# Performance work log

Measured on AMD Instinct MI355X. Metric: run time of the kernel, lower is better.

Reference implementation:

```python
import jax, jax.numpy as jnp
import numpy as np

NUM_CAV = 62000            # CAVs in the ragged batch
K = 3                      # past frames per object


def _counts():
    # deterministic ragged counts in [1, 31]; sum = 2000 * 496 = 992000 objects
    return ((np.arange(NUM_CAV) % 31) + 1).astype(np.int32)


def setup_inputs() -> dict:
    key = jax.random.key(0)
    k1, k2 = jax.random.split(key)
    counts = _counts()
    n_obj = int(counts.sum())  # 992000
    # [N, 3, 7] past 7-dof boxes; only [..., :2] (x, y) is used
    past_k_object_bbx = jax.random.normal(k1, (n_obj, K, 7), dtype=jnp.float32) * 10.0
    # strictly increasing timestamps per CAV so frame-to-frame dt != 0
    dt = jax.random.uniform(k2, (NUM_CAV, K), dtype=jnp.float32, minval=0.05, maxval=0.2)
    past_k_time_interval = jnp.cumsum(dt, axis=1).reshape(-1)  # flat, view(-1,3) compatible
    past_k_object_cav_num = jnp.asarray(counts)
    return {
        'past_k_object_bbx': past_k_object_bbx,
        'past_k_time_interval': past_k_time_interval,
        'past_k_object_cav_num': past_k_object_cav_num,
    }


def reference(past_k_object_bbx, past_k_time_interval, past_k_object_cav_num):
    # Faithful vectorization of extract_date_backup1 (j-indexed replicate loop ==
    # repeat_interleave of per-CAV time rows to per-object rows).
    n_obj = past_k_object_bbx.shape[0]
    # time grid per CAV, reversed so index -1 is the most recent frame
    td = jnp.flip(past_k_time_interval.reshape(-1, K), axis=1)        # [C, 3]
    coords = jnp.flip(past_k_object_bbx[:, :, :2], axis=1)           # [N, 3, 2]
    coords = coords - coords[:, -1:, :]                               # normalize to last frame
    # ragged row replication -> gather via cumulative offsets
    offsets = jnp.cumsum(past_k_object_cav_num)                       # [C]
    cav_idx = jnp.searchsorted(offsets, jnp.arange(n_obj), side='right')
    td_rep = td[cav_idx]                                              # [N, 3]
    td_norm = td_rep - td_rep[:, -1:]                                  # [N, 3]
    dt = td_rep[:, 1:] - td_rep[:, :-1]                                # [N, 2] (time_encode)
    distance = coords[:, 1:, :] - coords[:, :-1, :]                    # [N, 2, 2]
    speed = distance / dt[..., None]                                   # [N, 2, 2]
    obj_input = jnp.concatenate([distance, speed], axis=-1)[None]      # [1, N, 2, 4]
    # linear extrapolation of last motion to t = 0 (the 'query')
    last_len = td_norm[:, -1] - td_norm[:, -2]                          # [N]
    safe_len = jnp.where(last_len == 0, jnp.float32(1.0), last_len)
    extrap = coords[:, -1, :] + (coords[:, -1, :] - coords[:, -2, :]) * (-td_rep[:, -1:]) / safe_len[:, None]
    query = jnp.where((last_len == 0)[:, None], jnp.float32(0.0), extrap).reshape(1, n_obj, 1, 2)
    target_time_diff = -td_rep[:, -1]                                  # [N]
    time_encode = dt                                                   # [N, 2]
    return obj_input, query, time_encode, target_time_diff
```

## Files before the change

### kernel.cpp

```cpp
#include <hip/hip_runtime.h>
#include <limits.h>
#include <stdint.h>

#define SCAN_BS 1024
#define OBJ_PER 512
#define OBJ_BS  512
#define SLAB_F  (OBJ_PER * 21)
#define WIN     513
#define SOFF_CH 9

__device__ __forceinline__ void gload_lds16(const void* g, void* l) {
    __builtin_amdgcn_global_load_lds(
        (const __attribute__((address_space(1))) uint32_t*)g,
        (__attribute__((address_space(3))) uint32_t*)l, 16, 0, 0);
}
__device__ __forceinline__ void gload_lds4(const void* g, void* l) {
    __builtin_amdgcn_global_load_lds(
        (const __attribute__((address_space(1))) uint32_t*)g,
        (__attribute__((address_space(3))) uint32_t*)l, 4, 0, 0);
}


__global__ __launch_bounds__(SCAN_BS) void scan_fused_kernel(
    const int* __restrict__ counts, int C,
    int* __restrict__ flags, int* __restrict__ offsets, int* __restrict__ blockCav) {

    __shared__ int sdata[SCAN_BS];
    __shared__ int carry_s;
    const int b = blockIdx.x;
    const int tid = threadIdx.x;
    const int gid = b * SCAN_BS + tid;
    const int v = (gid < C) ? counts[gid] : 0;

    sdata[tid] = v;
    __syncthreads();
    for (int ofs = 1; ofs < SCAN_BS; ofs <<= 1) {
        int add = (tid >= ofs) ? sdata[tid - ofs] : 0;
        __syncthreads();
        sdata[tid] += add;
        __syncthreads();
    }

    if (tid == SCAN_BS - 1)
        __hip_atomic_store(&flags[b], sdata[SCAN_BS - 1] + 1,
                           __ATOMIC_RELEASE, __HIP_MEMORY_SCOPE_AGENT);

    if (tid < 64) {
        int sum = 0;
        for (int p = tid; p < b; p += 64) {
            int f;
            do {
                f = __hip_atomic_load(&flags[p], __ATOMIC_ACQUIRE, __HIP_MEMORY_SCOPE_AGENT);
            } while (f == 0);
            sum += f - 1;
        }
        #pragma unroll
        for (int o = 32; o > 0; o >>= 1) sum += __shfl_down(sum, o, 64);
        if (tid == 0) carry_s = sum;
    }
    __syncthreads();

    if (gid < C) {
        const int end = sdata[tid] + carry_s;
        offsets[gid] = end;
        const int start = end - v;
        int s0 = ((start + OBJ_PER - 1) / OBJ_PER) * OBJ_PER;
        for (int s = s0; s < end; s += OBJ_PER) blockCav[s / OBJ_PER] = gid;
    }
}


__global__ __launch_bounds__(OBJ_BS) void motion_kernel(
    const float* __restrict__ bbx, const float* __restrict__ tint,
    const int* __restrict__ offsets, const int* __restrict__ blockCav,
    int C, int N, float* __restrict__ out) {

    __shared__ __align__(16) float sb[SLAB_F];
    __shared__ int soff[SOFF_CH * 64];

    const int tid  = threadIdx.x;
    const int lane = tid & 63;
    const int wid  = tid >> 6;
    const long long blockStart = (long long)blockIdx.x * OBJ_PER;
    const int nObjBlk = (int)min((long long)OBJ_PER, (long long)N - blockStart);

    const int c_lo = blockCav[blockIdx.x];

    const float* gsrc = bbx + blockStart * 21;
    const int nBytes = nObjBlk * 84;
    const int nCh = nBytes >> 10;
    for (int ch = wid; ch < nCh; ch += 8)
        gload_lds16((const void*)(gsrc + ch * 256 + lane * 4), (void*)(sb + ch * 256));
    const int remF = (nBytes - (nCh << 10)) >> 2;
    for (int k = tid; k < remF; k += OBJ_BS) sb[nCh * 256 + k] = gsrc[nCh * 256 + k];

    int c0 = min(c_lo, C - WIN); if (c0 < 0) c0 = 0;
    if (wid == 0) {
        #pragma unroll
        for (int ch = 0; ch < SOFF_CH; ++ch)
            gload_lds4((const void*)(offsets + c0 + ch * 64 + lane), (void*)(soff + ch * 64));
    }

    __syncthreads();

    if (tid >= nObjBlk) return;
    const int i = (int)(blockStart + tid);

    int lo = 0, hi = WIN;
    while (lo < hi) {
        int mid = (lo + hi) >> 1;
        if (soff[mid] > i) hi = mid; else lo = mid + 1;
    }
    const int cav = c0 + lo;

    const float t0 = tint[3 * cav + 0];
    const float t1 = tint[3 * cav + 1];
    const float t2 = tint[3 * cav + 2];

    const float dt0 = t1 - t2;
    const float dt1 = t0 - t1;

    const float* b = sb + tid * 21;
    const float x0 = b[0],  y0 = b[1];
    const float x1 = b[7],  y1 = b[8];
    const float x2 = b[14], y2 = b[15];

    const float c0x = x2 - x0, c0y = y2 - y0;
    const float c1x = x1 - x0, c1y = y1 - y0;

    const float d0x = c1x - c0x, d0y = c1y - c0y;
    const float d1x = 0.0f - c1x, d1y = 0.0f - c1y;

    const float s0x = d0x / dt0, s0y = d0y / dt0;
    const float s1x = d1x / dt1, s1y = d1y / dt1;

    const float last_len = 0.0f - (t1 - t0);
    const float safe_len = (last_len == 0.0f) ? 1.0f : last_len;
    const float exx = ((0.0f - c1x) * (0.0f - t0)) / safe_len;
    const float exy = ((0.0f - c1y) * (0.0f - t0)) / safe_len;
    const float qx = (last_len == 0.0f) ? 0.0f : exx;
    const float qy = (last_len == 0.0f) ? 0.0f : exy;

    const size_t Ns = (size_t)N;
    float4* oi = (float4*)out;
    oi[(size_t)i * 2 + 0] = make_float4(d0x, d0y, s0x, s0y);
    oi[(size_t)i * 2 + 1] = make_float4(d1x, d1y, s1x, s1y);

    float2* q  = (float2*)(out + 8 * Ns);
    q[i] = make_float2(qx, qy);

    float2* te = (float2*)(out + 10 * Ns);
    te[i] = make_float2(dt0, dt1);

    out[12 * Ns + (size_t)i] = 0.0f - t0;
}


extern "C" void kernel_launch(void* const* d_in, const int* in_sizes, int n_in,
                              void* d_out, int out_size, void* d_ws, size_t ws_size,
                              hipStream_t stream) {
    const float* bbx  = (const float*)d_in[0];
    const float* tint = (const float*)d_in[1];
    const int*   cnt  = (const int*)d_in[2];
    float* out = (float*)d_out;

    const int N = in_sizes[0] / 21;
    const int C = in_sizes[2];

    const int nb  = (C + SCAN_BS - 1) / SCAN_BS;
    const int nob = (N + OBJ_PER - 1) / OBJ_PER;

    int* flags    = (int*)d_ws;
    int* offsets  = flags + ((nb + 63) & ~63);
    int* blockCav = offsets + C + 128;

    hipMemsetAsync(flags, 0, nb * sizeof(int), stream);
    scan_fused_kernel<<<nb, SCAN_BS, 0, stream>>>(cnt, C, flags, offsets, blockCav);
    motion_kernel<<<nob, OBJ_BS, 0, stream>>>(bbx, tint, offsets, blockCav, C, N, out);
}
```

Measured before the change: 41.89 us.

## Replace decoupled-lookback scan with redundant prefix sum; shrink motion blocks to 256

The scan kernel no longer publishes per-block flags and spin-waits on earlier blocks. Each block now sums all preceding counts directly from global memory, which removes the memset launch and the inter-block dependency chain. In exchange the redundant reads grow quadratically with block count, though with about 61 blocks this is small. Separately, the motion kernel moves to 256-object blocks for more blocks and a smaller LDS footprint, with a full-tile fast path that issues a fixed number of LDS-direct loads.

```diff
diff --git a/kernel.cpp b/kernel.cpp
--- a/kernel.cpp
+++ b/kernel.cpp
@@ -1,13 +1,12 @@
 #include <hip/hip_runtime.h>
-#include <limits.h>
 #include <stdint.h>
 
 #define SCAN_BS 1024
-#define OBJ_PER 512
-#define OBJ_BS  512
-#define SLAB_F  (OBJ_PER * 21)
-#define WIN     513
-#define SOFF_CH 9
+#define OBJ_BS  256
+#define SLAB_F  (OBJ_BS * 21)
+#define SLAB_CH (SLAB_F / 256)
+#define WIN     257
+#define SOFF_CH 5
 
 __device__ __forceinline__ void gload_lds16(const void* g, void* l) {
     __builtin_amdgcn_global_load_lds(
@@ -23,17 +22,28 @@
 
 __global__ __launch_bounds__(SCAN_BS) void scan_fused_kernel(
     const int* __restrict__ counts, int C,
-    int* __restrict__ flags, int* __restrict__ offsets, int* __restrict__ blockCav) {
+    int* __restrict__ offsets, int* __restrict__ blockCav) {
 
     __shared__ int sdata[SCAN_BS];
-    __shared__ int carry_s;
-    const int b = blockIdx.x;
-    const int tid = threadIdx.x;
-    const int gid = b * SCAN_BS + tid;
+    __shared__ int wsum[SCAN_BS / 64];
+
+    const int tid  = threadIdx.x;
+    const int lane = tid & 63;
+    const int wid  = tid >> 6;
+    const int b    = blockIdx.x;
+    const int gid  = b * SCAN_BS + tid;
+    const int chunkStart = b * SCAN_BS;
+
     const int v = (gid < C) ? counts[gid] : 0;
+    sdata[tid] = v;
 
-    sdata[tid] = v;
+    int csum = 0;
+    for (int idx = tid; idx < chunkStart; idx += SCAN_BS) csum += counts[idx];
+    #pragma unroll
+    for (int o = 32; o > 0; o >>= 1) csum += __shfl_down(csum, o, 64);
+    if (lane == 0) wsum[wid] = csum;
     __syncthreads();
+
     for (int ofs = 1; ofs < SCAN_BS; ofs <<= 1) {
         int add = (tid >= ofs) ? sdata[tid - ofs] : 0;
         __syncthreads();
@@ -41,31 +51,16 @@
         __syncthreads();
     }
 
-    if (tid == SCAN_BS - 1)
-        __hip_atomic_store(&flags[b], sdata[SCAN_BS - 1] + 1,
-                           __ATOMIC_RELEASE, __HIP_MEMORY_SCOPE_AGENT);
-
-    if (tid < 64) {
-        int sum = 0;
-        for (int p = tid; p < b; p += 64) {
-            int f;
-            do {
-                f = __hip_atomic_load(&flags[p], __ATOMIC_ACQUIRE, __HIP_MEMORY_SCOPE_AGENT);
-            } while (f == 0);
-            sum += f - 1;
-        }
-        #pragma unroll
-        for (int o = 32; o > 0; o >>= 1) sum += __shfl_down(sum, o, 64);
-        if (tid == 0) carry_s = sum;
-    }
-    __syncthreads();
+    int carry = 0;
+    #pragma unroll
+    for (int w = 0; w < SCAN_BS / 64; ++w) carry += wsum[w];
 
     if (gid < C) {
-        const int end = sdata[tid] + carry_s;
+        const int end = sdata[tid] + carry;
         offsets[gid] = end;
         const int start = end - v;
-        int s0 = ((start + OBJ_PER - 1) / OBJ_PER) * OBJ_PER;
-        for (int s = s0; s < end; s += OBJ_PER) blockCav[s / OBJ_PER] = gid;
+        int s0 = ((start + OBJ_BS - 1) / OBJ_BS) * OBJ_BS;
+        for (int s = s0; s < end; s += OBJ_BS) blockCav[s / OBJ_BS] = gid;
     }
 }
 
@@ -81,18 +76,20 @@
     const int tid  = threadIdx.x;
     const int lane = tid & 63;
     const int wid  = tid >> 6;
-    const long long blockStart = (long long)blockIdx.x * OBJ_PER;
-    const int nObjBlk = (int)min((long long)OBJ_PER, (long long)N - blockStart);
+    const long long blockStart = (long long)blockIdx.x * OBJ_BS;
+    const int nObjBlk = (int)min((long long)OBJ_BS, (long long)N - blockStart);
 
     const int c_lo = blockCav[blockIdx.x];
 
     const float* gsrc = bbx + blockStart * 21;
-    const int nBytes = nObjBlk * 84;
-    const int nCh = nBytes >> 10;
-    for (int ch = wid; ch < nCh; ch += 8)
-        gload_lds16((const void*)(gsrc + ch * 256 + lane * 4), (void*)(sb + ch * 256));
-    const int remF = (nBytes - (nCh << 10)) >> 2;
-    for (int k = tid; k < remF; k += OBJ_BS) sb[nCh * 256 + k] = gsrc[nCh * 256 + k];
+    if (nObjBlk == OBJ_BS) {
+        #pragma unroll
+        for (int ch = wid; ch < SLAB_CH; ch += 4)
+            gload_lds16((const void*)(gsrc + ch * 256 + lane * 4), (void*)(sb + ch * 256));
+    } else {
+        const int nElem = nObjBlk * 21;
+        for (int k = tid; k < nElem; k += OBJ_BS) sb[k] = gsrc[k];
+    }
 
     int c0 = min(c_lo, C - WIN); if (c0 < 0) c0 = 0;
     if (wid == 0) {
@@ -120,10 +117,10 @@
     const float dt0 = t1 - t2;
     const float dt1 = t0 - t1;
 
-    const float* b = sb + tid * 21;
-    const float x0 = b[0],  y0 = b[1];
-    const float x1 = b[7],  y1 = b[8];
-    const float x2 = b[14], y2 = b[15];
+    const float* bp = sb + tid * 21;
+    const float x0 = bp[0],  y0 = bp[1];
+    const float x1 = bp[7],  y1 = bp[8];
+    const float x2 = bp[14], y2 = bp[15];
 
     const float c0x = x2 - x0, c0y = y2 - y0;
     const float c1x = x1 - x0, c1y = y1 - y0;
@@ -168,13 +165,11 @@
     const int C = in_sizes[2];
 
     const int nb  = (C + SCAN_BS - 1) / SCAN_BS;
-    const int nob = (N + OBJ_PER - 1) / OBJ_PER;
+    const int nob = (N + OBJ_BS - 1) / OBJ_BS;
 
-    int* flags    = (int*)d_ws;
-    int* offsets  = flags + ((nb + 63) & ~63);
-    int* blockCav = offsets + C + 128;
+    int* offsets  = (int*)d_ws;
+    int* blockCav = offsets + C + 64;
 
-    hipMemsetAsync(flags, 0, nb * sizeof(int), stream);
-    scan_fused_kernel<<<nb, SCAN_BS, 0, stream>>>(cnt, C, flags, offsets, blockCav);
+    scan_fused_kernel<<<nb, SCAN_BS, 0, stream>>>(cnt, C, offsets, blockCav);
     motion_kernel<<<nob, OBJ_BS, 0, stream>>>(bbx, tint, offsets, blockCav, C, N, out);
 }
```

After: 38.89 us. 1.08x faster.
